# Kernel optimization log

Hardware: AMD Instinct MI355X
Metric: run time of the kernel (lower is better)

The kernel has to match this reference:

```python
import jax, jax.numpy as jnp
import numpy as np

N_QUBITS = 14
N_LAYERS = 6
BATCH = 1024

# ---- gate constructors (PennyLane conventions) ----

def _rx(t):
    # RX(t) = [[cos t/2, -i sin t/2], [-i sin t/2, cos t/2]]
    tc = t.astype(jnp.complex64)
    c = jnp.cos(tc / 2)
    s = jnp.sin(tc / 2)
    return jnp.stack([jnp.stack([c, -1j * s]), jnp.stack([-1j * s, c])])


def _rz(t):
    # RZ(t) = diag(e^{-it/2}, e^{+it/2})
    e = jnp.exp(-1j * t.astype(jnp.complex64) / 2)
    z = jnp.zeros_like(e)
    return jnp.stack([jnp.stack([e, z]), jnp.stack([z, jnp.conj(e)])])


def _ry(t):
    c = jnp.cos(t / 2)
    s = jnp.sin(t / 2)
    return jnp.stack([jnp.stack([c, -s]), jnp.stack([s, c])]).astype(jnp.complex64)


def _rot(phi, theta, omega):
    # PennyLane Rot(phi, theta, omega) = RZ(omega) @ RY(theta) @ RZ(phi)
    return _rz(omega) @ _ry(theta) @ _rz(phi)


# ---- state-vector gate application (state shape: (2,)*n) ----

def _apply_1q(state, gate, w):
    s = jnp.moveaxis(state, w, 0)          # (2, 2^{n-1} view)
    s = jnp.tensordot(gate, s, axes=([1], [0]))
    return jnp.moveaxis(s, 0, w)


def _apply_cnot(state, c, t):
    s = jnp.moveaxis(state, (c, t), (0, 1))  # (2_control, 2_target, ...)
    s = s.at[1].set(s[1, ::-1])              # flip target where control==1
    return jnp.moveaxis(s, (0, 1), (c, t))


def _simulate(xi, weights):
    n = N_QUBITS
    state = jnp.zeros((2,) * n, jnp.complex64).at[(0,) * n].set(1.0)
    # angle encoding: RX(x_i) on wire i
    for w in range(n):
        state = _apply_1q(state, _rx(xi[w]), w)
    # StronglyEntanglingLayers: Rot on every wire, then CNOT ring with range r
    for l in range(N_LAYERS):
        for w in range(n):
            g = _rot(weights[l, w, 0], weights[l, w, 1], weights[l, w, 2])
            state = _apply_1q(state, g, w)
        r = (l % (n - 1)) + 1  # PennyLane default ranges
        for w in range(n):
            state = _apply_cnot(state, w, (w + r) % n)
    # <Z_0> = P(q0=0) - P(q0=1)
    p = jnp.abs(state.reshape(2, -1)) ** 2
    return jnp.sum(p[0]) - jnp.sum(p[1])


def setup_inputs() -> dict:
    key = jax.random.key(0)
    k1, k2 = jax.random.split(key)
    x = jax.random.normal(k1, (BATCH, N_QUBITS), dtype=jnp.float32)
    weights = 0.01 * jax.random.normal(k2, (N_LAYERS, N_QUBITS, 3), dtype=jnp.float32)
    return {"x": x, "weights": weights}


def reference(x, weights):
    # x: (B, n_qubits) angles -> (B,) expectation values of PauliZ on wire 0
    return jax.vmap(lambda xi: _simulate(xi, weights))(x)
```

## Files before the change

### kernel.cpp

```cpp
#include <hip/hip_runtime.h>
#include <hip/hip_fp16.h>
#include <math.h>

#define NQ 14
#define NL 6
#define NT 512
#define BATCH 1024
#define NGATES (NL * NQ)
#define GINIT 0x111


typedef _Float16 half8 __attribute__((ext_vector_type(8)));
typedef float f32x16 __attribute__((ext_vector_type(16)));

__device__ constexpr int ring_F(int l, int v) {
    int r = (l % 13) + 1;
    for (int w = 0; w < NQ; ++w) {
        int pc = 13 - w, pt = 13 - ((w + r) % NQ);
        v ^= ((v >> pc) & 1) << pt;
    }
    return v;
}

__device__ constexpr int gcorr(int G, int a, int p) {
    int keys = (a & 15) | ((p & 1) << 4);
    int c = 0;
    for (int k = 0; k < 5; ++k) if ((keys >> k) & 1) c ^= (G >> (3 * k)) & 7;
    return c;
}
__device__ constexpr int lam0(int a, int p, int G) {
    int chunk = ((a >> 4) & 31) | (((a >> 12) & 1) << 5) | (((a >> 13) & 1) << 6)
              | ((p & 1) << 7) | ((a & 15) << 8);
    chunk ^= gcorr(G, a, p);
    return ((a >> 9) & 7) | (chunk << 3);
}
__device__ constexpr int lam1(int a, int p) {
    int chunk = (a & 15) | (((a >> 13) & 1) << 4) | (((a >> 7) & 1) << 5)
              | (((a >> 8) & 1) << 6) | ((p & 1) << 7) | (((a >> 12) & 1) << 8)
              | (((a >> 9) & 7) << 9);
    chunk ^= (a >> 9) & 7;
    return ((a >> 4) & 7) | (chunk << 3);
}
__device__ constexpr int lam2(int a, int p) {
    int chunk = ((a >> 9) & 31) | (((a >> 3) & 1) << 5) | ((p & 1) << 6)
              | (((a >> 7) & 3) << 7) | (((a >> 4) & 7) << 9);
    chunk ^= (a >> 4) & 7;
    return (a & 7) | (chunk << 3);
}

__device__ constexpr int vrank5(int v0, int v1, int v2, int v3, int v4, int v5) {
    int vs[6] = {v0, v1, v2, v3, v4, v5};
    int basis[5] = {0, 0, 0, 0, 0};
    int r = 0;
    for (int i = 0; i < 6; ++i) {
        int x = vs[i];
        for (int b = 4; b >= 0; --b) {
            if (((x >> b) & 1) == 0) continue;
            if (basis[b]) { x ^= basis[b]; }
            else { basis[b] = x; ++r; break; }
        }
    }
    return r;
}
__device__ constexpr int scat_rank(int L, int G) {
    return vrank5(
        (lam0(ring_F(L, 1), 0, G) >> 1) & 31,
        (lam0(ring_F(L, 2), 0, G) >> 1) & 31,
        (lam0(ring_F(L, 4), 0, G) >> 1) & 31,
        (lam0(ring_F(L, 8), 0, G) >> 1) & 31,
        (lam0(0, 1, G) >> 1) & 31,
        (lam0(ring_F(L, 1 << 11), 0, G) >> 1) & 31);
}
__device__ constexpr int find_g0(int L) {
    if (scat_rank(L, GINIT) == 5) return GINIT;
    for (int s = 0; s < 15; ++s)
        if (scat_rank(L, GINIT ^ (1 << s)) == 5) return GINIT ^ (1 << s);
    for (int s1 = 0; s1 < 15; ++s1)
        for (int s2 = s1 + 1; s2 < 15; ++s2)
            if (scat_rank(L, GINIT ^ (1 << s1) ^ (1 << s2)) == 5)
                return GINIT ^ (1 << s1) ^ (1 << s2);
    int best = GINIT, br = scat_rank(L, GINIT);
    for (int s = 0; s < 15; ++s) {
        int g = GINIT ^ (1 << s);
        int rr = scat_rank(L, g);
        if (rr > br) { best = g; br = rr; }
    }
    return best;
}
__device__ constexpr int gsrc(int L) { return L < 0 ? GINIT : find_g0(L); }

__global__ void prep_kernel(const float* __restrict__ wts, float* __restrict__ gm) {
    int g = blockIdx.x * blockDim.x + threadIdx.x;
    if (g < NGATES) {
        float phi = wts[g*3+0], th = wts[g*3+1], om = wts[g*3+2];
        float c = cosf(0.5f*th), s = sinf(0.5f*th);
        float a = 0.5f*(phi+om), bb = 0.5f*(phi-om);
        float ca = cosf(a), sa = sinf(a);
        float cb = cosf(bb), sb = sinf(bb);
        gm[g*8+0] = c*ca;  gm[g*8+1] = -c*sa;
        gm[g*8+2] = -s*cb; gm[g*8+3] = -s*sb;
        gm[g*8+4] = s*cb;  gm[g*8+5] = -s*sb;
        gm[g*8+6] = c*ca;  gm[g*8+7] = c*sa;
    }
}

__global__ void prep2_kernel(const float* __restrict__ gm, _Float16* __restrict__ B) {
    int t = blockIdx.x * blockDim.x + threadIdx.x;
    if (t >= NL * 18 * 64) return;
    int lane = t & 63;
    int fi = (t >> 6) % 18;
    int L = t / (18 * 64);
    int a, tt, m;
    if (fi < 8)       { a = 0; tt = fi >> 2;        m = fi & 3; }
    else if (fi < 16) { a = 1; tt = (fi - 8) >> 2;  m = (fi - 8) & 3; }
    else              { a = 2; tt = 0;              m = fi - 16; }
    int h = lane >> 5, c = lane & 31;
    for (int e = 0; e < 8; ++e) {
        int kc, kp, nc, np, nb;
        if (a < 2) { int kr = 16*m + 8*h + e; int nr = 32*tt + c;
                     kc = kr & 31; kp = kr >> 5; nc = nr & 31; np = nr >> 5; nb = 5; }
        else       { kc = 8*h + e; kp = m; nc = c & 15; np = c >> 4; nb = 4; }
        float gr = 1.f, gi = 0.f;
        for (int j = 0; j < nb; ++j) {
            int w = (a == 0) ? (4 - j) : (a == 1) ? (9 - j) : (13 - j);
            const float* mm = gm + (L*NQ + w)*8;
            const float* ent = mm + (((nc >> j) & 1) * 2 + ((kc >> j) & 1)) * 2;
            float er = ent[0], ei = ent[1];
            float ngr = gr*er - gi*ei, ngi = gr*ei + gi*er;
            gr = ngr; gi = ngi;
        }
        float v = (kp == np) ? gr : (kp ? -gi : gi);
        B[((L*18 + fi)*64 + lane)*8 + e] = (_Float16)v;
    }
}

template<int L>
__device__ __forceinline__ void apply0(_Float16* st, const _Float16* B,
                                       int lane, int l31, int h, int w) {
    constexpr int GR = gsrc(L - 1);
    half8 Af[2][4];
    const int rb = lam0(w | (l31 << 4) | (h << 12), 0, GR);
    #pragma unroll
    for (int ss = 0; ss < 2; ++ss)
        #pragma unroll
        for (int m = 0; m < 4; ++m)
            Af[ss][m] = *(const half8*)(st + (rb ^ lam0((ss << 3) | ((m & 1) << 13), m >> 1, GR)));
    __syncthreads();
    half8 Bf[8];
    #pragma unroll
    for (int f = 0; f < 8; ++f)
        Bf[f] = *(const half8*)(B + ((L*18 + f)*64 + lane)*8);
    const int wb = lam1(w | (h << 6) | (l31 << 9), 0);
    #pragma unroll
    for (int ss = 0; ss < 2; ++ss)
        #pragma unroll
        for (int t = 0; t < 2; ++t) {
            f32x16 acc;
            #pragma unroll
            for (int j = 0; j < 16; ++j) acc[j] = 0.f;
            #pragma unroll
            for (int m = 0; m < 4; ++m)
                acc = __builtin_amdgcn_mfma_f32_32x32x16_f16(Af[ss][m], Bf[t*4+m], acc, 0, 0, 0);
            #pragma unroll
            for (int q = 0; q < 4; ++q) {
                uint2 wv;
                wv.x = __builtin_bit_cast(unsigned, __builtin_amdgcn_cvt_pkrtz(acc[4*q+0], acc[4*q+1]));
                wv.y = __builtin_bit_cast(unsigned, __builtin_amdgcn_cvt_pkrtz(acc[4*q+2], acc[4*q+3]));
                *(uint2*)(st + (wb ^ lam1((ss << 3) | ((q & 1) << 7) | ((q >> 1) << 8), t))) = wv;
            }
        }
    __syncthreads();
}

template<int L>
__device__ __forceinline__ void apply1(_Float16* st, const _Float16* B,
                                       int lane, int l31, int h, int w) {
    half8 Af[2][4];
    const int rb = lam1((l31 & 15) | (h << 7) | (w << 9) | (((l31 >> 4) & 1) << 13), 0);
    #pragma unroll
    for (int ss = 0; ss < 2; ++ss)
        #pragma unroll
        for (int m = 0; m < 4; ++m)
            Af[ss][m] = *(const half8*)(st + (rb ^ lam1((ss << 12) | ((m & 1) << 8), m >> 1)));
    __syncthreads();
    half8 Bf[8];
    #pragma unroll
    for (int f = 0; f < 8; ++f)
        Bf[f] = *(const half8*)(B + ((L*18 + 8 + f)*64 + lane)*8);
    const int wb = lam2((h << 2) | (l31 << 4) | (w << 9), 0);
    #pragma unroll
    for (int ss = 0; ss < 2; ++ss)
        #pragma unroll
        for (int t = 0; t < 2; ++t) {
            f32x16 acc;
            #pragma unroll
            for (int j = 0; j < 16; ++j) acc[j] = 0.f;
            #pragma unroll
            for (int m = 0; m < 4; ++m)
                acc = __builtin_amdgcn_mfma_f32_32x32x16_f16(Af[ss][m], Bf[t*4+m], acc, 0, 0, 0);
            #pragma unroll
            for (int q = 0; q < 4; ++q) {
                uint2 wv;
                wv.x = __builtin_bit_cast(unsigned, __builtin_amdgcn_cvt_pkrtz(acc[4*q+0], acc[4*q+1]));
                wv.y = __builtin_bit_cast(unsigned, __builtin_amdgcn_cvt_pkrtz(acc[4*q+2], acc[4*q+3]));
                *(uint2*)(st + (wb ^ lam2((ss << 12) | ((q & 1) << 3) | ((q >> 1) << 13), t))) = wv;
            }
        }
    __syncthreads();
}

template<int L>
__device__ __forceinline__ void apply2(_Float16* st, const _Float16* B,
                                       int lane, int l31, int h, int w) {
    constexpr int GW = find_g0(L);
    half8 Af[4][2];
    const int rb = lam2((h << 3) | (w << 4) | (l31 << 9), 0);
    #pragma unroll
    for (int ss = 0; ss < 4; ++ss)
        #pragma unroll
        for (int m = 0; m < 2; ++m)
            Af[ss][m] = *(const half8*)(st + (rb ^ lam2(ss << 7, m)));
    __syncthreads();
    half8 Bf[2];
    #pragma unroll
    for (int f = 0; f < 2; ++f)
        Bf[f] = *(const half8*)(B + ((L*18 + 16 + f)*64 + lane)*8);
    constexpr int C0 = lam0(ring_F(L, 1), 0, GW);
    constexpr int C1 = lam0(ring_F(L, 2), 0, GW);
    constexpr int C2 = lam0(ring_F(L, 4), 0, GW);
    constexpr int C3 = lam0(ring_F(L, 8), 0, GW);
    constexpr int CP = lam0(0, 1, GW);
    constexpr int CH = lam0(ring_F(L, 1 << 11), 0, GW);
    constexpr int CW0 = lam0(ring_F(L, 1 << 4), 0, GW);
    constexpr int CW1 = lam0(ring_F(L, 1 << 5), 0, GW);
    constexpr int CW2 = lam0(ring_F(L, 1 << 6), 0, GW);
    constexpr int CS0 = lam0(ring_F(L, 1 << 7), 0, GW);
    constexpr int CS1 = lam0(ring_F(L, 1 << 8), 0, GW);
    constexpr int E9  = lam0(ring_F(L, 1 << 9), 0, GW);
    constexpr int E10 = lam0(ring_F(L, 1 << 10), 0, GW);
    constexpr int E12 = lam0(ring_F(L, 1 << 12), 0, GW);
    constexpr int E13 = lam0(ring_F(L, 1 << 13), 0, GW);
    int wb = ((l31 & 1) ? C0 : 0) ^ ((l31 & 2) ? C1 : 0) ^ ((l31 & 4) ? C2 : 0)
           ^ ((l31 & 8) ? C3 : 0) ^ ((l31 & 16) ? CP : 0) ^ (h ? CH : 0)
           ^ ((w & 1) ? CW0 : 0) ^ ((w & 2) ? CW1 : 0) ^ ((w & 4) ? CW2 : 0);
    #pragma unroll
    for (int ss = 0; ss < 4; ++ss) {
        f32x16 acc;
        #pragma unroll
        for (int j = 0; j < 16; ++j) acc[j] = 0.f;
        acc = __builtin_amdgcn_mfma_f32_32x32x16_f16(Af[ss][0], Bf[0], acc, 0, 0, 0);
        acc = __builtin_amdgcn_mfma_f32_32x32x16_f16(Af[ss][1], Bf[1], acc, 0, 0, 0);
        const int ws_ = wb ^ ((ss & 1) ? CS0 : 0) ^ ((ss & 2) ? CS1 : 0);
        #pragma unroll
        for (int r = 0; r < 16; ++r) {
            int wa = ws_ ^ ((r & 1) ? E9 : 0) ^ ((r & 2) ? E10 : 0)
                         ^ ((r & 4) ? E12 : 0) ^ ((r & 8) ? E13 : 0);
            st[wa] = (_Float16)acc[r];
        }
    }
    __syncthreads();
}

template<int L>
__device__ __forceinline__ void do_layer(_Float16* st, const _Float16* B,
                                         int lane, int l31, int h, int w) {
    apply0<L>(st, B, lane, l31, h, w);
    apply1<L>(st, B, lane, l31, h, w);
    apply2<L>(st, B, lane, l31, h, w);
    if constexpr (L < NL - 1) do_layer<L+1>(st, B, lane, l31, h, w);
}

__global__ void __launch_bounds__(NT, 4)
qsim_kernel(const float* __restrict__ x, const _Float16* __restrict__ B,
            float* __restrict__ out)
{
    __shared__ _Float16 st[32768];
    const int tid = threadIdx.x;
    const int lane = tid & 63, wid = tid >> 6;
    const int l31 = lane & 31, h = lane >> 5;
    const float* xb = x + blockIdx.x * NQ;

    {
        float cr = 1.f, ci = 0.f;
        #pragma unroll
        for (int bb = 0; bb < 3; ++bb) {
            float s, c; __sincosf(0.5f * xb[13 - bb], &s, &c);
            if ((wid >> bb) & 1) { float nr = s*ci, ni = -s*cr; cr = nr; ci = ni; }
            else                 { cr *= c; ci *= c; }
        }
        {
            float s, c; __sincosf(0.5f * xb[10], &s, &c);
            if (h) { float nr = s*ci, ni = -s*cr; cr = nr; ci = ni; }
            else   { cr *= c; ci *= c; }
        }
        #pragma unroll
        for (int bb = 0; bb < 5; ++bb) {
            float s, c; __sincosf(0.5f * xb[9 - bb], &s, &c);
            if ((l31 >> bb) & 1) { float nr = s*ci, ni = -s*cr; cr = nr; ci = ni; }
            else                 { cr *= c; ci *= c; }
        }
        float es[3], ec[3];
        #pragma unroll
        for (int bb = 0; bb < 3; ++bb) __sincosf(0.5f * xb[4 - bb], &es[bb], &ec[bb]);
        float s1, c1, s0, c0;
        __sincosf(0.5f * xb[1], &s1, &c1);
        __sincosf(0.5f * xb[0], &s0, &c0);
        const int ib = lam0(wid | (h << 3) | (l31 << 4), 0, GINIT);
        #pragma unroll
        for (int j2 = 0; j2 < 4; ++j2) {
            float dr = cr, di = ci;
            if (j2 & 1) { float nr = s1*di, ni = -s1*dr; dr = nr; di = ni; }
            else        { dr *= c1; di *= c1; }
            if (j2 >> 1) { float nr = s0*di, ni = -s0*dr; dr = nr; di = ni; }
            else         { dr *= c0; di *= c0; }
            half8 R, I;
            #pragma unroll
            for (int e = 0; e < 8; ++e) {
                float rr = dr, ii = di;
                #pragma unroll
                for (int bb = 0; bb < 3; ++bb) {
                    if ((e >> bb) & 1) { float nr = es[bb]*ii, ni = -es[bb]*rr; rr = nr; ii = ni; }
                    else               { rr *= ec[bb]; ii *= ec[bb]; }
                }
                R[e] = (_Float16)rr; I[e] = (_Float16)ii;
            }
            int da = ((j2 & 1) << 12) | ((j2 >> 1) << 13);
            *(half8*)(st + (ib ^ lam0(da, 0, GINIT))) = R;
            *(half8*)(st + (ib ^ lam0(da, 1, GINIT))) = I;
        }
    }
    __syncthreads();

    do_layer<0>(st, B, lane, l31, h, wid);

    {
        constexpr int G5 = find_g0(NL - 1);
        const int rb = lam0(wid | (l31 << 4) | (h << 12), 0, G5);
        float acc = 0.f;
        #pragma unroll
        for (int ss = 0; ss < 2; ++ss)
            #pragma unroll
            for (int m0 = 0; m0 < 2; ++m0) {
                half8 re = *(const half8*)(st + (rb ^ lam0((ss << 3) | (m0 << 13), 0, G5)));
                half8 im = *(const half8*)(st + (rb ^ lam0((ss << 3) | (m0 << 13), 1, G5)));
                float s = 0.f;
                #pragma unroll
                for (int e = 0; e < 8; ++e) {
                    float r = (float)re[e], iv = (float)im[e];
                    s += r*r + iv*iv;
                }
                acc += m0 ? -s : s;
            }
        #pragma unroll
        for (int off = 32; off > 0; off >>= 1) acc += __shfl_down(acc, off, 64);
        __syncthreads();
        float* f = (float*)st;
        if ((tid & 63) == 0) f[tid >> 6] = acc;
        __syncthreads();
        if (tid == 0) {
            float s = 0.f;
            #pragma unroll
            for (int w = 0; w < NT/64; ++w) s += f[w];
            out[blockIdx.x] = s;
        }
    }
}

extern "C" void kernel_launch(void* const* d_in, const int* in_sizes, int n_in,
                              void* d_out, int out_size, void* d_ws, size_t ws_size,
                              hipStream_t stream) {
    const float* x = (const float*)d_in[0];
    const float* w = (const float*)d_in[1];
    float* out = (float*)d_out;
    float* gm = (float*)d_ws;
    _Float16* B = (_Float16*)((char*)d_ws + 4096);

    prep_kernel<<<1, 128, 0, stream>>>(w, gm);
    prep2_kernel<<<27, 256, 0, stream>>>(gm, B);
    qsim_kernel<<<BATCH, NT, 0, stream>>>(x, B, out);
}
```

Before: 146.5 us.

## Double threads per circuit block and fuse gate-matrix prep kernels

Raises the block size to 1024 threads, so each wave handles half as many state-vector sub-tiles per gate stage. The ss loops are folded into the wave index in the apply stages, the initial encoding and the readout. B fragments are now loaded right next to each MFMA instead of preloaded, which cuts register pressure to fit the launch bound of 8. The two prep kernels are merged into one, removing a launch and the intermediate gate-matrix buffer. The cost is more threads contending at each __syncthreads and redundant trig work per thread in the prep kernel.

Result: slower. 178.5 us (+21.8%).

```diff
diff --git a/kernel.cpp b/kernel.cpp
--- a/kernel.cpp
+++ b/kernel.cpp
@@ -4,7 +4,7 @@
 
 #define NQ 14
 #define NL 6
-#define NT 512
+#define NT 1024
 #define BATCH 1024
 #define NGATES (NL * NQ)
 #define GINIT 0x111
@@ -89,22 +89,7 @@
 }
 __device__ constexpr int gsrc(int L) { return L < 0 ? GINIT : find_g0(L); }
 
-__global__ void prep_kernel(const float* __restrict__ wts, float* __restrict__ gm) {
-    int g = blockIdx.x * blockDim.x + threadIdx.x;
-    if (g < NGATES) {
-        float phi = wts[g*3+0], th = wts[g*3+1], om = wts[g*3+2];
-        float c = cosf(0.5f*th), s = sinf(0.5f*th);
-        float a = 0.5f*(phi+om), bb = 0.5f*(phi-om);
-        float ca = cosf(a), sa = sinf(a);
-        float cb = cosf(bb), sb = sinf(bb);
-        gm[g*8+0] = c*ca;  gm[g*8+1] = -c*sa;
-        gm[g*8+2] = -s*cb; gm[g*8+3] = -s*sb;
-        gm[g*8+4] = s*cb;  gm[g*8+5] = -s*sb;
-        gm[g*8+6] = c*ca;  gm[g*8+7] = c*sa;
-    }
-}
-
-__global__ void prep2_kernel(const float* __restrict__ gm, _Float16* __restrict__ B) {
+__global__ void prepB_kernel(const float* __restrict__ wts, _Float16* __restrict__ B) {
     int t = blockIdx.x * blockDim.x + threadIdx.x;
     if (t >= NL * 18 * 64) return;
     int lane = t & 63;
@@ -115,19 +100,39 @@
     else if (fi < 16) { a = 1; tt = (fi - 8) >> 2;  m = (fi - 8) & 3; }
     else              { a = 2; tt = 0;              m = fi - 16; }
     int h = lane >> 5, c = lane & 31;
+    const int nb = (a < 2) ? 5 : 4;
+    float gmat[5][8];
+    #pragma unroll
+    for (int j = 0; j < 5; ++j) {
+        if (j < nb) {
+            int w = (a == 0) ? (4 - j) : (a == 1) ? (9 - j) : (13 - j);
+            int g = L * NQ + w;
+            float phi = wts[g*3+0], th = wts[g*3+1], om = wts[g*3+2];
+            float cc = cosf(0.5f*th), sn = sinf(0.5f*th);
+            float aa = 0.5f*(phi+om), bb = 0.5f*(phi-om);
+            float ca = cosf(aa), sa = sinf(aa);
+            float cb = cosf(bb), sb = sinf(bb);
+            gmat[j][0] = cc*ca;  gmat[j][1] = -cc*sa;
+            gmat[j][2] = -sn*cb; gmat[j][3] = -sn*sb;
+            gmat[j][4] = sn*cb;  gmat[j][5] = -sn*sb;
+            gmat[j][6] = cc*ca;  gmat[j][7] = cc*sa;
+        }
+    }
+    #pragma unroll
     for (int e = 0; e < 8; ++e) {
-        int kc, kp, nc, np, nb;
+        int kc, kp, nc, np;
         if (a < 2) { int kr = 16*m + 8*h + e; int nr = 32*tt + c;
-                     kc = kr & 31; kp = kr >> 5; nc = nr & 31; np = nr >> 5; nb = 5; }
-        else       { kc = 8*h + e; kp = m; nc = c & 15; np = c >> 4; nb = 4; }
+                     kc = kr & 31; kp = kr >> 5; nc = nr & 31; np = nr >> 5; }
+        else       { kc = 8*h + e; kp = m; nc = c & 15; np = c >> 4; }
         float gr = 1.f, gi = 0.f;
-        for (int j = 0; j < nb; ++j) {
-            int w = (a == 0) ? (4 - j) : (a == 1) ? (9 - j) : (13 - j);
-            const float* mm = gm + (L*NQ + w)*8;
-            const float* ent = mm + (((nc >> j) & 1) * 2 + ((kc >> j) & 1)) * 2;
-            float er = ent[0], ei = ent[1];
-            float ngr = gr*er - gi*ei, ngi = gr*ei + gi*er;
-            gr = ngr; gi = ngi;
+        #pragma unroll
+        for (int j = 0; j < 5; ++j) {
+            if (j < nb) {
+                const float* ent = &gmat[j][(((nc >> j) & 1) * 2 + ((kc >> j) & 1)) * 2];
+                float er = ent[0], ei = ent[1];
+                float ngr = gr*er - gi*ei, ngi = gr*ei + gi*er;
+                gr = ngr; gi = ngi;
+            }
         }
         float v = (kp == np) ? gr : (kp ? -gi : gi);
         B[((L*18 + fi)*64 + lane)*8 + e] = (_Float16)v;
@@ -138,74 +143,63 @@
 __device__ __forceinline__ void apply0(_Float16* st, const _Float16* B,
                                        int lane, int l31, int h, int w) {
     constexpr int GR = gsrc(L - 1);
-    half8 Af[2][4];
+    half8 Af[4];
     const int rb = lam0(w | (l31 << 4) | (h << 12), 0, GR);
     #pragma unroll
-    for (int ss = 0; ss < 2; ++ss)
-        #pragma unroll
-        for (int m = 0; m < 4; ++m)
-            Af[ss][m] = *(const half8*)(st + (rb ^ lam0((ss << 3) | ((m & 1) << 13), m >> 1, GR)));
-    __syncthreads();
-    half8 Bf[8];
-    #pragma unroll
-    for (int f = 0; f < 8; ++f)
-        Bf[f] = *(const half8*)(B + ((L*18 + f)*64 + lane)*8);
+    for (int m = 0; m < 4; ++m)
+        Af[m] = *(const half8*)(st + (rb ^ lam0((m & 1) << 13, m >> 1, GR)));
+    __syncthreads();
     const int wb = lam1(w | (h << 6) | (l31 << 9), 0);
     #pragma unroll
-    for (int ss = 0; ss < 2; ++ss)
-        #pragma unroll
-        for (int t = 0; t < 2; ++t) {
-            f32x16 acc;
-            #pragma unroll
-            for (int j = 0; j < 16; ++j) acc[j] = 0.f;
-            #pragma unroll
-            for (int m = 0; m < 4; ++m)
-                acc = __builtin_amdgcn_mfma_f32_32x32x16_f16(Af[ss][m], Bf[t*4+m], acc, 0, 0, 0);
-            #pragma unroll
-            for (int q = 0; q < 4; ++q) {
-                uint2 wv;
-                wv.x = __builtin_bit_cast(unsigned, __builtin_amdgcn_cvt_pkrtz(acc[4*q+0], acc[4*q+1]));
-                wv.y = __builtin_bit_cast(unsigned, __builtin_amdgcn_cvt_pkrtz(acc[4*q+2], acc[4*q+3]));
-                *(uint2*)(st + (wb ^ lam1((ss << 3) | ((q & 1) << 7) | ((q >> 1) << 8), t))) = wv;
-            }
-        }
+    for (int t = 0; t < 2; ++t) {
+        f32x16 acc;
+        #pragma unroll
+        for (int j = 0; j < 16; ++j) acc[j] = 0.f;
+        #pragma unroll
+        for (int m = 0; m < 4; ++m) {
+            half8 Bf = *(const half8*)(B + ((L*18 + t*4 + m)*64 + lane)*8);
+            acc = __builtin_amdgcn_mfma_f32_32x32x16_f16(Af[m], Bf, acc, 0, 0, 0);
+        }
+        #pragma unroll
+        for (int q = 0; q < 4; ++q) {
+            uint2 wv;
+            wv.x = __builtin_bit_cast(unsigned, __builtin_amdgcn_cvt_pkrtz(acc[4*q+0], acc[4*q+1]));
+            wv.y = __builtin_bit_cast(unsigned, __builtin_amdgcn_cvt_pkrtz(acc[4*q+2], acc[4*q+3]));
+            *(uint2*)(st + (wb ^ lam1(((q & 1) << 7) | ((q >> 1) << 8), t))) = wv;
+        }
+    }
     __syncthreads();
 }
 
 template<int L>
 __device__ __forceinline__ void apply1(_Float16* st, const _Float16* B,
                                        int lane, int l31, int h, int w) {
-    half8 Af[2][4];
-    const int rb = lam1((l31 & 15) | (h << 7) | (w << 9) | (((l31 >> 4) & 1) << 13), 0);
-    #pragma unroll
-    for (int ss = 0; ss < 2; ++ss)
-        #pragma unroll
-        for (int m = 0; m < 4; ++m)
-            Af[ss][m] = *(const half8*)(st + (rb ^ lam1((ss << 12) | ((m & 1) << 8), m >> 1)));
-    __syncthreads();
-    half8 Bf[8];
-    #pragma unroll
-    for (int f = 0; f < 8; ++f)
-        Bf[f] = *(const half8*)(B + ((L*18 + 8 + f)*64 + lane)*8);
-    const int wb = lam2((h << 2) | (l31 << 4) | (w << 9), 0);
-    #pragma unroll
-    for (int ss = 0; ss < 2; ++ss)
-        #pragma unroll
-        for (int t = 0; t < 2; ++t) {
-            f32x16 acc;
-            #pragma unroll
-            for (int j = 0; j < 16; ++j) acc[j] = 0.f;
-            #pragma unroll
-            for (int m = 0; m < 4; ++m)
-                acc = __builtin_amdgcn_mfma_f32_32x32x16_f16(Af[ss][m], Bf[t*4+m], acc, 0, 0, 0);
-            #pragma unroll
-            for (int q = 0; q < 4; ++q) {
-                uint2 wv;
-                wv.x = __builtin_bit_cast(unsigned, __builtin_amdgcn_cvt_pkrtz(acc[4*q+0], acc[4*q+1]));
-                wv.y = __builtin_bit_cast(unsigned, __builtin_amdgcn_cvt_pkrtz(acc[4*q+2], acc[4*q+3]));
-                *(uint2*)(st + (wb ^ lam2((ss << 12) | ((q & 1) << 3) | ((q >> 1) << 13), t))) = wv;
-            }
-        }
+    half8 Af[4];
+    const int rb = lam1((l31 & 15) | (h << 7) | ((w & 7) << 9) | ((w >> 3) << 12)
+                        | (((l31 >> 4) & 1) << 13), 0);
+    #pragma unroll
+    for (int m = 0; m < 4; ++m)
+        Af[m] = *(const half8*)(st + (rb ^ lam1((m & 1) << 8, m >> 1)));
+    __syncthreads();
+    const int wb = lam2((h << 2) | (l31 << 4) | ((w & 7) << 9) | ((w >> 3) << 12), 0);
+    #pragma unroll
+    for (int t = 0; t < 2; ++t) {
+        f32x16 acc;
+        #pragma unroll
+        for (int j = 0; j < 16; ++j) acc[j] = 0.f;
+        #pragma unroll
+        for (int m = 0; m < 4; ++m) {
+            half8 Bf = *(const half8*)(B + ((L*18 + 8 + t*4 + m)*64 + lane)*8);
+            acc = __builtin_amdgcn_mfma_f32_32x32x16_f16(Af[m], Bf, acc, 0, 0, 0);
+        }
+        #pragma unroll
+        for (int q = 0; q < 4; ++q) {
+            uint2 wv;
+            wv.x = __builtin_bit_cast(unsigned, __builtin_amdgcn_cvt_pkrtz(acc[4*q+0], acc[4*q+1]));
+            wv.y = __builtin_bit_cast(unsigned, __builtin_amdgcn_cvt_pkrtz(acc[4*q+2], acc[4*q+3]));
+            *(uint2*)(st + (wb ^ lam2(((q & 1) << 3) | ((q >> 1) << 13), t))) = wv;
+        }
+    }
     __syncthreads();
 }
 
@@ -213,13 +207,13 @@
 __device__ __forceinline__ void apply2(_Float16* st, const _Float16* B,
                                        int lane, int l31, int h, int w) {
     constexpr int GW = find_g0(L);
-    half8 Af[4][2];
+    half8 Af[2][2];
     const int rb = lam2((h << 3) | (w << 4) | (l31 << 9), 0);
     #pragma unroll
-    for (int ss = 0; ss < 4; ++ss)
+    for (int ss = 0; ss < 2; ++ss)
         #pragma unroll
         for (int m = 0; m < 2; ++m)
-            Af[ss][m] = *(const half8*)(st + (rb ^ lam2(ss << 7, m)));
+            Af[ss][m] = *(const half8*)(st + (rb ^ lam2(ss << 8, m)));
     __syncthreads();
     half8 Bf[2];
     #pragma unroll
@@ -242,15 +236,16 @@
     constexpr int E13 = lam0(ring_F(L, 1 << 13), 0, GW);
     int wb = ((l31 & 1) ? C0 : 0) ^ ((l31 & 2) ? C1 : 0) ^ ((l31 & 4) ? C2 : 0)
            ^ ((l31 & 8) ? C3 : 0) ^ ((l31 & 16) ? CP : 0) ^ (h ? CH : 0)
-           ^ ((w & 1) ? CW0 : 0) ^ ((w & 2) ? CW1 : 0) ^ ((w & 4) ? CW2 : 0);
-    #pragma unroll
-    for (int ss = 0; ss < 4; ++ss) {
+           ^ ((w & 1) ? CW0 : 0) ^ ((w & 2) ? CW1 : 0) ^ ((w & 4) ? CW2 : 0)
+           ^ ((w & 8) ? CS0 : 0);
+    #pragma unroll
+    for (int ss = 0; ss < 2; ++ss) {
         f32x16 acc;
         #pragma unroll
         for (int j = 0; j < 16; ++j) acc[j] = 0.f;
         acc = __builtin_amdgcn_mfma_f32_32x32x16_f16(Af[ss][0], Bf[0], acc, 0, 0, 0);
         acc = __builtin_amdgcn_mfma_f32_32x32x16_f16(Af[ss][1], Bf[1], acc, 0, 0, 0);
-        const int ws_ = wb ^ ((ss & 1) ? CS0 : 0) ^ ((ss & 2) ? CS1 : 0);
+        const int ws_ = wb ^ (ss ? CS1 : 0);
         #pragma unroll
         for (int r = 0; r < 16; ++r) {
             int wa = ws_ ^ ((r & 1) ? E9 : 0) ^ ((r & 2) ? E10 : 0)
@@ -270,7 +265,7 @@
     if constexpr (L < NL - 1) do_layer<L+1>(st, B, lane, l31, h, w);
 }
 
-__global__ void __launch_bounds__(NT, 4)
+__global__ void __launch_bounds__(NT, 8)
 qsim_kernel(const float* __restrict__ x, const _Float16* __restrict__ B,
             float* __restrict__ out)
 {
@@ -290,8 +285,8 @@
         }
         {
             float s, c; __sincosf(0.5f * xb[10], &s, &c);
-            if (h) { float nr = s*ci, ni = -s*cr; cr = nr; ci = ni; }
-            else   { cr *= c; ci *= c; }
+            if (wid >> 3) { float nr = s*ci, ni = -s*cr; cr = nr; ci = ni; }
+            else          { cr *= c; ci *= c; }
         }
         #pragma unroll
         for (int bb = 0; bb < 5; ++bb) {
@@ -299,20 +294,22 @@
             if ((l31 >> bb) & 1) { float nr = s*ci, ni = -s*cr; cr = nr; ci = ni; }
             else                 { cr *= c; ci *= c; }
         }
+        {
+            float s, c; __sincosf(0.5f * xb[1], &s, &c);
+            if (h) { float nr = s*ci, ni = -s*cr; cr = nr; ci = ni; }
+            else   { cr *= c; ci *= c; }
+        }
         float es[3], ec[3];
         #pragma unroll
         for (int bb = 0; bb < 3; ++bb) __sincosf(0.5f * xb[4 - bb], &es[bb], &ec[bb]);
-        float s1, c1, s0, c0;
-        __sincosf(0.5f * xb[1], &s1, &c1);
+        float s0, c0;
         __sincosf(0.5f * xb[0], &s0, &c0);
-        const int ib = lam0(wid | (h << 3) | (l31 << 4), 0, GINIT);
-        #pragma unroll
-        for (int j2 = 0; j2 < 4; ++j2) {
+        const int ib = lam0(wid | (l31 << 4) | (h << 12), 0, GINIT);
+        #pragma unroll
+        for (int j2 = 0; j2 < 2; ++j2) {
             float dr = cr, di = ci;
-            if (j2 & 1) { float nr = s1*di, ni = -s1*dr; dr = nr; di = ni; }
-            else        { dr *= c1; di *= c1; }
-            if (j2 >> 1) { float nr = s0*di, ni = -s0*dr; dr = nr; di = ni; }
-            else         { dr *= c0; di *= c0; }
+            if (j2) { float nr = s0*di, ni = -s0*dr; dr = nr; di = ni; }
+            else    { dr *= c0; di *= c0; }
             half8 R, I;
             #pragma unroll
             for (int e = 0; e < 8; ++e) {
@@ -324,9 +321,8 @@
                 }
                 R[e] = (_Float16)rr; I[e] = (_Float16)ii;
             }
-            int da = ((j2 & 1) << 12) | ((j2 >> 1) << 13);
-            *(half8*)(st + (ib ^ lam0(da, 0, GINIT))) = R;
-            *(half8*)(st + (ib ^ lam0(da, 1, GINIT))) = I;
+            *(half8*)(st + (ib ^ lam0(j2 << 13, 0, GINIT))) = R;
+            *(half8*)(st + (ib ^ lam0(j2 << 13, 1, GINIT))) = I;
         }
     }
     __syncthreads();
@@ -338,19 +334,17 @@
         const int rb = lam0(wid | (l31 << 4) | (h << 12), 0, G5);
         float acc = 0.f;
         #pragma unroll
-        for (int ss = 0; ss < 2; ++ss)
+        for (int m0 = 0; m0 < 2; ++m0) {
+            half8 re = *(const half8*)(st + (rb ^ lam0(m0 << 13, 0, G5)));
+            half8 im = *(const half8*)(st + (rb ^ lam0(m0 << 13, 1, G5)));
+            float s = 0.f;
             #pragma unroll
-            for (int m0 = 0; m0 < 2; ++m0) {
-                half8 re = *(const half8*)(st + (rb ^ lam0((ss << 3) | (m0 << 13), 0, G5)));
-                half8 im = *(const half8*)(st + (rb ^ lam0((ss << 3) | (m0 << 13), 1, G5)));
-                float s = 0.f;
-                #pragma unroll
-                for (int e = 0; e < 8; ++e) {
-                    float r = (float)re[e], iv = (float)im[e];
-                    s += r*r + iv*iv;
-                }
-                acc += m0 ? -s : s;
+            for (int e = 0; e < 8; ++e) {
+                float r = (float)re[e], iv = (float)im[e];
+                s += r*r + iv*iv;
             }
+            acc += m0 ? -s : s;
+        }
         #pragma unroll
         for (int off = 32; off > 0; off >>= 1) acc += __shfl_down(acc, off, 64);
         __syncthreads();
@@ -372,10 +366,8 @@
     const float* x = (const float*)d_in[0];
     const float* w = (const float*)d_in[1];
     float* out = (float*)d_out;
-    float* gm = (float*)d_ws;
-    _Float16* B = (_Float16*)((char*)d_ws + 4096);
-
-    prep_kernel<<<1, 128, 0, stream>>>(w, gm);
-    prep2_kernel<<<27, 256, 0, stream>>>(gm, B);
+    _Float16* B = (_Float16*)d_ws;
+
+    prepB_kernel<<<27, 256, 0, stream>>>(w, B);
     qsim_kernel<<<BATCH, NT, 0, stream>>>(x, B, out);
 }
```
